# Kernel optimization log

Hardware: AMD Instinct MI355X
Metric: run time of the kernel (lower is better)

The kernel has to match this reference:

```python
import jax, jax.numpy as jnp
import numpy as np

B, S, D, H = 2, 2048, 1024, 16
HD = D // H  # head_dim = 64


def setup_inputs() -> dict:
    key = jax.random.key(0)
    ks = jax.random.split(key, 9)
    s = 1.0 / np.sqrt(D)
    return {
        "x": jax.random.normal(ks[0], (B, S, D), dtype=jnp.float32),
        "Wq": jax.random.uniform(ks[1], (D, D), jnp.float32, -s, s),
        "bq": jnp.zeros((D,), jnp.float32),
        "Wk": jax.random.uniform(ks[2], (D, D), jnp.float32, -s, s),
        "bk": jnp.zeros((D,), jnp.float32),
        "Wv": jax.random.uniform(ks[3], (D, D), jnp.float32, -s, s),
        "bv": jnp.zeros((D,), jnp.float32),
        "Wo": jax.random.uniform(ks[4], (D, D), jnp.float32, -s, s),
        "bo": jnp.zeros((D,), jnp.float32),
    }


def reference(x, Wq, bq, Wk, bk, Wv, bv, Wo, bo):
    # x: [B,S,D] -> Q/K/V: [B,H,S,HD]
    def heads(t):
        return t.reshape(B, S, H, HD).transpose(0, 2, 1, 3)

    Q = heads(x @ Wq + bq)
    K = heads(x @ Wk + bk)
    V = heads(x @ Wv + bv)
    scale = jnp.sqrt(jnp.asarray(HD, dtype=x.dtype))
    energy = jnp.einsum("bhqd,bhkd->bhqk", Q, K) / scale  # [B,H,S,S]
    attn = jax.nn.softmax(energy, axis=-1)
    # dropout is identity in eval mode
    o = jnp.einsum("bhqk,bhkd->bhqd", attn, V)  # [B,H,S,HD]
    o = o.transpose(0, 2, 1, 3).reshape(B, S, D)
    return o @ Wo + bo
```

## Files before the change

### kernel.cpp

```cpp
#include <hip/hip_runtime.h>
#include <hip/hip_bf16.h>

#define B_  2
#define S_  2048
#define D_  1024
#define H_  16
#define HD_ 64

typedef __attribute__((ext_vector_type(8))) short bf16x8;
typedef __attribute__((ext_vector_type(4))) short bf16x4;
typedef __attribute__((ext_vector_type(4))) float f32x4;

typedef __attribute__((address_space(1))) const short gbl_short;
typedef __attribute__((address_space(3))) short lds_short;

__device__ __forceinline__ short f2bf(float f) {
  union { float f; unsigned u; } v; v.f = f;
  unsigned r = (v.u + 0x7FFFu + ((v.u >> 16) & 1u)) >> 16;
  return (short)r;
}

__device__ __forceinline__ short bf16s(float f) {
  __hip_bfloat16 h = __float2bfloat16(f);
  return *reinterpret_cast<short*>(&h);
}

__global__ __launch_bounds__(256) void cast_x_kernel(const float* __restrict__ x,
                                                     short* __restrict__ xb) {
  int i = blockIdx.x * 256 + threadIdx.x;
  float4 v = ((const float4*)x)[i];
  short4 o;
  o.x = f2bf(v.x); o.y = f2bf(v.y); o.z = f2bf(v.z); o.w = f2bf(v.w);
  ((short4*)xb)[i] = o;
}

__global__ __launch_bounds__(256) void transpose_cast_w(
    const float* __restrict__ w0, const float* __restrict__ w1,
    const float* __restrict__ w2, const float* __restrict__ w3,
    short* __restrict__ t0, short* __restrict__ t1,
    short* __restrict__ t2, short* __restrict__ t3) {
  const float* W = blockIdx.z == 0 ? w0 : blockIdx.z == 1 ? w1 : blockIdx.z == 2 ? w2 : w3;
  short* T       = blockIdx.z == 0 ? t0 : blockIdx.z == 1 ? t1 : blockIdx.z == 2 ? t2 : t3;
  __shared__ float tile[32][33];
  int tx = threadIdx.x, ty = threadIdx.y;
  int x0 = blockIdx.x * 32, y0 = blockIdx.y * 32;
#pragma unroll
  for (int i = 0; i < 4; ++i)
    tile[ty + i * 8][tx] = W[(y0 + ty + i * 8) * D_ + x0 + tx];
  __syncthreads();
#pragma unroll
  for (int i = 0; i < 4; ++i)
    T[(x0 + ty + i * 8) * D_ + y0 + tx] = f2bf(tile[tx][ty + i * 8]);
}

__global__ __launch_bounds__(256) void qkv_gemm(
    const short* __restrict__ xb,
    const short* __restrict__ Wqt, const short* __restrict__ Wkt, const short* __restrict__ Wvt,
    const float* __restrict__ bq, const float* __restrict__ bk, const float* __restrict__ bv,
    short* __restrict__ Qb, short* __restrict__ Kb, short* __restrict__ Vtb) {
  const int which = blockIdx.z;
  const short* Bt   = which == 0 ? Wqt : which == 1 ? Wkt : Wvt;
  const float* bias = which == 0 ? bq  : which == 1 ? bk  : bv;
  const float scl   = which == 0 ? 0.125f * 1.44269504089f : 1.0f;
  const int lane = threadIdx.x & 63, wave = threadIdx.x >> 6;
  const int l15 = lane & 15, quad = lane >> 4;
  const int wm = wave & 1, wn = wave >> 1;
  const int m0 = blockIdx.x * 128, n0 = blockIdx.y * 128;
  const int srow = lane >> 2;
  const int skp  = (lane & 3) * 8;

  __shared__ short lA[2][128 * 32];
  __shared__ short lB[2][128 * 32];

  f32x4 acc[4][4];
#pragma unroll
  for (int mi = 0; mi < 4; ++mi)
#pragma unroll
    for (int ni = 0; ni < 4; ++ni) { f32x4 z = {0.f, 0.f, 0.f, 0.f}; acc[mi][ni] = z; }

  auto stage = [&](int it, int buf) {
    int kk = it * 32;
#pragma unroll
    for (int j = 0; j < 2; ++j) {
      int c = wave * 2 + j;
      int row = c * 16 + srow;
      __builtin_amdgcn_global_load_lds(
          (gbl_short*)(xb + (m0 + row) * D_ + kk + skp),
          (lds_short*)(&lA[buf][0] + c * 512 + lane * 8), 16, 0, 0);
      __builtin_amdgcn_global_load_lds(
          (gbl_short*)(Bt + (n0 + row) * D_ + kk + skp),
          (lds_short*)(&lB[buf][0] + c * 512 + lane * 8), 16, 0, 0);
    }
  };

  stage(0, 0);
  __syncthreads();
  for (int it = 0; it < 32; ++it) {
    int cur = it & 1;
    if (it < 31) stage(it + 1, cur ^ 1);
    bf16x8 af[4], bf[4];
#pragma unroll
    for (int i = 0; i < 4; ++i) {
      af[i] = *(const bf16x8*)(&lA[cur][0] + (wm * 64 + i * 16 + l15) * 32 + quad * 8);
      bf[i] = *(const bf16x8*)(&lB[cur][0] + (wn * 64 + i * 16 + l15) * 32 + quad * 8);
    }
#pragma unroll
    for (int mi = 0; mi < 4; ++mi)
#pragma unroll
      for (int ni = 0; ni < 4; ++ni)
        acc[mi][ni] = __builtin_amdgcn_mfma_f32_16x16x32_bf16(af[mi], bf[ni], acc[mi][ni], 0, 0, 0);
    if (it < 31) __syncthreads();
  }

#pragma unroll
  for (int mi = 0; mi < 4; ++mi) {
    int m = m0 + wm * 64 + mi * 16 + quad * 4;
    int bb = m >> 11;
    int s0 = m & (S_ - 1);
#pragma unroll
    for (int ni = 0; ni < 4; ++ni) {
      int n = n0 + wn * 64 + ni * 16 + l15;
      int h = n >> 6, hd = n & 63;
      float bsv = bias[n];
      if (which < 2) {
        short* dst = which == 0 ? Qb : Kb;
#pragma unroll
        for (int r = 0; r < 4; ++r)
          dst[((bb * H_ + h) * S_ + (s0 + r)) * HD_ + hd] = f2bf((acc[mi][ni][r] + bsv) * scl);
      } else {
        short4 pk;
        pk.x = f2bf(acc[mi][ni][0] + bsv);
        pk.y = f2bf(acc[mi][ni][1] + bsv);
        pk.z = f2bf(acc[mi][ni][2] + bsv);
        pk.w = f2bf(acc[mi][ni][3] + bsv);
        *(short4*)(Vtb + ((bb * H_ + h) * HD_ + hd) * S_ + s0) = pk;
      }
    }
  }
}

__global__ __launch_bounds__(256) void out_gemm(
    const short* __restrict__ Ob, const short* __restrict__ Wot,
    const float* __restrict__ bo, float* __restrict__ out) {
  const int lane = threadIdx.x & 63, wave = threadIdx.x >> 6;
  const int l15 = lane & 15, quad = lane >> 4;
  const int m0 = blockIdx.x * 128, n0 = blockIdx.y * 64;
  const int srow = lane >> 2;
  const int skp  = (lane & 3) * 8;

  __shared__ short lA[2][128 * 32];
  __shared__ short lB[2][64 * 32];

  f32x4 acc[2][4];
#pragma unroll
  for (int mi = 0; mi < 2; ++mi)
#pragma unroll
    for (int ni = 0; ni < 4; ++ni) { f32x4 z = {0.f, 0.f, 0.f, 0.f}; acc[mi][ni] = z; }

  auto stage = [&](int it, int buf) {
    int kk = it * 32;
#pragma unroll
    for (int j = 0; j < 2; ++j) {
      int c = wave * 2 + j;
      __builtin_amdgcn_global_load_lds(
          (gbl_short*)(Ob + (m0 + c * 16 + srow) * D_ + kk + skp),
          (lds_short*)(&lA[buf][0] + c * 512 + lane * 8), 16, 0, 0);
    }
    __builtin_amdgcn_global_load_lds(
        (gbl_short*)(Wot + (n0 + wave * 16 + srow) * D_ + kk + skp),
        (lds_short*)(&lB[buf][0] + wave * 512 + lane * 8), 16, 0, 0);
  };

  stage(0, 0);
  __syncthreads();
  for (int it = 0; it < 32; ++it) {
    int cur = it & 1;
    if (it < 31) stage(it + 1, cur ^ 1);
    bf16x8 af[2], bf[4];
#pragma unroll
    for (int i = 0; i < 2; ++i)
      af[i] = *(const bf16x8*)(&lA[cur][0] + (wave * 32 + i * 16 + l15) * 32 + quad * 8);
#pragma unroll
    for (int i = 0; i < 4; ++i)
      bf[i] = *(const bf16x8*)(&lB[cur][0] + (i * 16 + l15) * 32 + quad * 8);
#pragma unroll
    for (int mi = 0; mi < 2; ++mi)
#pragma unroll
      for (int ni = 0; ni < 4; ++ni)
        acc[mi][ni] = __builtin_amdgcn_mfma_f32_16x16x32_bf16(af[mi], bf[ni], acc[mi][ni], 0, 0, 0);
    if (it < 31) __syncthreads();
  }

#pragma unroll
  for (int mi = 0; mi < 2; ++mi) {
    int m = m0 + wave * 32 + mi * 16 + quad * 4;
#pragma unroll
    for (int ni = 0; ni < 4; ++ni) {
      int n = n0 + ni * 16 + l15;
      float bsv = bo[n];
#pragma unroll
      for (int r = 0; r < 4; ++r)
        out[(m + r) * D_ + n] = acc[mi][ni][r] + bsv;
    }
  }
}

__global__ __launch_bounds__(256, 2) void attn_kernel(
    const short* __restrict__ Qb, const short* __restrict__ Kb,
    const short* __restrict__ Vtb, short* __restrict__ Ob) {
  const int qt = blockIdx.x, h = blockIdx.y, b = blockIdx.z;
  const int base = (b * H_ + h) * S_ * HD_;
  const int tid = threadIdx.x;
  const int lane = tid & 63, wave = tid >> 6;
  const int grp = wave >> 1;
  const int wq  = wave & 1;
  const int l15 = lane & 15, quad = lane >> 4;

  __shared__ __align__(16) char smem[33280];
  short* lK = (short*)smem;
  short* lV = (short*)(smem + 16384);

  const int q0 = qt * 128 + wq * 64;

  bf16x8 qf[4][2];
#pragma unroll
  for (int mi = 0; mi < 4; ++mi)
#pragma unroll
    for (int ks = 0; ks < 2; ++ks)
      qf[mi][ks] = *(const bf16x8*)(Qb + base + (q0 + mi * 16 + l15) * HD_ + ks * 32 + quad * 8);

  f32x4 oacc[4][4];
  f32x4 lacc[4];
#pragma unroll
  for (int mi = 0; mi < 4; ++mi) {
    f32x4 z = {0.f, 0.f, 0.f, 0.f};
    lacc[mi] = z;
#pragma unroll
    for (int nb = 0; nb < 4; ++nb) oacc[mi][nb] = z;
  }

  bf16x8 onesf;
#pragma unroll
  for (int i = 0; i < 8; ++i) onesf[i] = (short)0x3F80;

  const int tig = tid & 127;
  const int slotK = tig & 7,  rowK = tig >> 3;
  const int slotV = tig & 3,  rowV = tig >> 2;
  const short* kp = Kb + base + (grp * 1024 + rowK) * HD_ + ((slotK ^ (rowK & 7)) * 8);
  const short* vp = Vtb + base + rowV * S_ + grp * 1024 + ((slotV ^ ((rowV >> 2) & 3)) * 8);
  lds_short* ldk = (lds_short*)(lK + grp * 2048 + tig * 8);
  lds_short* ldv = (lds_short*)(lV + grp * 2048 + tig * 8);

  auto stage = [&](int kt, int buf) {
#pragma unroll
    for (int j = 0; j < 2; ++j) {
      __builtin_amdgcn_global_load_lds((gbl_short*)(kp + kt * 32 * HD_ + j * 16 * HD_),
                                       ldk + buf * 4096 + j * 1024, 16, 0, 0);
      __builtin_amdgcn_global_load_lds((gbl_short*)(vp + kt * 32 + j * 32 * S_),
                                       ldv + buf * 4096 + j * 1024, 16, 0, 0);
    }
  };

  const int swzK = l15 & 7;
  const int fsw  = (l15 >> 2) & 3;
  const int g1 = (quad >> 1) ^ fsw;
  const int g2 = (2 | (quad >> 1)) ^ fsw;
  const int vsub = (quad & 1) * 4;

  stage(0, 0);
  __syncthreads();

  for (int kt = 0; kt < 32; ++kt) {
    const int buf = kt & 1;
    if (kt < 31) stage(kt + 1, buf ^ 1);

    const short* lKc = lK + buf * 4096 + grp * 2048;
    const short* lVc = lV + buf * 4096 + grp * 2048;

    f32x4 sacc[4][2];
#pragma unroll
    for (int mi = 0; mi < 4; ++mi)
#pragma unroll
      for (int nb = 0; nb < 2; ++nb) { f32x4 z = {0.f, 0.f, 0.f, 0.f}; sacc[mi][nb] = z; }
#pragma unroll
    for (int nb = 0; nb < 2; ++nb)
#pragma unroll
      for (int ks = 0; ks < 2; ++ks) {
        bf16x8 kf = *(const bf16x8*)(lKc + (nb * 16 + l15) * 64 + (((ks * 4 + quad) ^ swzK) * 8));
#pragma unroll
        for (int mi = 0; mi < 4; ++mi)
          sacc[mi][nb] = __builtin_amdgcn_mfma_f32_16x16x32_bf16(kf, qf[mi][ks], sacc[mi][nb], 0, 0, 0);
      }

    bf16x8 af[4];
#pragma unroll
    for (int mi = 0; mi < 4; ++mi)
#pragma unroll
      for (int j = 0; j < 8; ++j)
        af[mi][j] = bf16s(__builtin_amdgcn_exp2f(sacc[mi][j >> 2][j & 3]));

#pragma unroll
    for (int nbh = 0; nbh < 4; ++nbh) {
      const short* vrow = lVc + (nbh * 16 + l15) * 32 + vsub;
      bf16x4 v1 = *(const bf16x4*)(vrow + g1 * 8);
      bf16x4 v2 = *(const bf16x4*)(vrow + g2 * 8);
      bf16x8 vf = __builtin_shufflevector(v1, v2, 0, 1, 2, 3, 4, 5, 6, 7);
#pragma unroll
      for (int mi = 0; mi < 4; ++mi)
        oacc[mi][nbh] = __builtin_amdgcn_mfma_f32_16x16x32_bf16(af[mi], vf, oacc[mi][nbh], 0, 0, 0);
    }
#pragma unroll
    for (int mi = 0; mi < 4; ++mi)
      lacc[mi] = __builtin_amdgcn_mfma_f32_16x16x32_bf16(af[mi], onesf, lacc[mi], 0, 0, 0);
    __syncthreads();
  }

  float* exch = (float*)smem;
  float* lex  = (float*)(smem + 32768);
  if (grp == 1) {
#pragma unroll
    for (int mi = 0; mi < 4; ++mi)
#pragma unroll
      for (int nbh = 0; nbh < 4; ++nbh)
#pragma unroll
        for (int r = 0; r < 4; ++r)
          exch[wq * 4096 + (mi * 16 + quad * 4 + r) * 64 + nbh * 16 + l15] = oacc[mi][nbh][r];
    if (l15 == 0) {
#pragma unroll
      for (int mi = 0; mi < 4; ++mi)
#pragma unroll
        for (int r = 0; r < 4; ++r)
          lex[wq * 64 + mi * 16 + quad * 4 + r] = lacc[mi][r];
    }
  }
  __syncthreads();
  if (grp == 0) {
#pragma unroll
    for (int mi = 0; mi < 4; ++mi)
#pragma unroll
      for (int r = 0; r < 4; ++r) {
        int row = mi * 16 + quad * 4 + r;
        float l2 = lex[wq * 64 + row];
        float inv = 1.0f / (lacc[mi][r] + l2);
        int sg = q0 + row;
#pragma unroll
        for (int nbh = 0; nbh < 4; ++nbh) {
          float o2 = exch[wq * 4096 + row * 64 + nbh * 16 + l15];
          Ob[(b * S_ + sg) * D_ + h * HD_ + nbh * 16 + l15] =
              bf16s((oacc[mi][nbh][r] + o2) * inv);
        }
      }
  }
}

extern "C" void kernel_launch(void* const* d_in, const int* in_sizes, int n_in,
                              void* d_out, int out_size, void* d_ws, size_t ws_size,
                              hipStream_t stream) {
  (void)in_sizes; (void)n_in; (void)out_size; (void)ws_size;
  const float* x  = (const float*)d_in[0];
  const float* Wq = (const float*)d_in[1];
  const float* bq = (const float*)d_in[2];
  const float* Wk = (const float*)d_in[3];
  const float* bk = (const float*)d_in[4];
  const float* Wv = (const float*)d_in[5];
  const float* bv = (const float*)d_in[6];
  const float* Wo = (const float*)d_in[7];
  const float* bo = (const float*)d_in[8];
  float* out = (float*)d_out;

  char* ws = (char*)d_ws;
  short* xb  = (short*)(ws);
  short* Wqt = (short*)(ws + 8388608);
  short* Wkt = Wqt + 1048576;
  short* Wvt = Wkt + 1048576;
  short* Wot = Wvt + 1048576;
  short* Qb  = Wot + 1048576;
  short* Kb  = Qb + 4194304;
  short* Vtb = Kb + 4194304;
  short* Ob  = Vtb + 4194304;

  cast_x_kernel<<<4096, 256, 0, stream>>>(x, xb);
  transpose_cast_w<<<dim3(32, 32, 4), dim3(32, 8), 0, stream>>>(
      Wq, Wk, Wv, Wo, Wqt, Wkt, Wvt, Wot);
  qkv_gemm<<<dim3(32, 8, 3), 256, 0, stream>>>(
      xb, Wqt, Wkt, Wvt, bq, bk, bv, Qb, Kb, Vtb);
  attn_kernel<<<dim3(16, 16, 2), 256, 0, stream>>>(Qb, Kb, Vtb, Ob);
  out_gemm<<<dim3(32, 16), 256, 0, stream>>>(Ob, Wot, bo, out);
}
```

Measured before the change: 193.6 us.

## Triple-buffer GEMM LDS stages with XOR swizzle and enlarge out_gemm tile

Both projection GEMMs move from double-buffered LDS staging with __syncthreads to a three-stage ring. Explicit vmcnt waits and raw barriers let two loads stay in flight while compute runs. The k-chunk column index is XOR-swizzled by row bits on write and read to reduce LDS bank conflicts on the 16-byte fragment reads. out_gemm switches from 128x64 to 128x128 tiles with a 2x2 wave layout, which halves its grid and increases reuse. This costs more LDS per block and lower occupancy, and correctness now depends on the hand-counted vmcnt values.

```diff
diff --git a/kernel.cpp b/kernel.cpp
--- a/kernel.cpp
+++ b/kernel.cpp
@@ -67,10 +67,11 @@
   const int wm = wave & 1, wn = wave >> 1;
   const int m0 = blockIdx.x * 128, n0 = blockIdx.y * 128;
   const int srow = lane >> 2;
-  const int skp  = (lane & 3) * 8;
-
-  __shared__ short lA[2][128 * 32];
-  __shared__ short lB[2][128 * 32];
+  const int skp  = (((lane & 3) ^ ((srow >> 1) & 3)) * 8);
+  const int rsw  = (l15 >> 1) & 3;
+
+  __shared__ short lA[3][128 * 32];
+  __shared__ short lB[3][128 * 32];
 
   f32x4 acc[4][4];
 #pragma unroll
@@ -93,24 +94,36 @@
     }
   };
 
-  stage(0, 0);
-  __syncthreads();
-  for (int it = 0; it < 32; ++it) {
-    int cur = it & 1;
-    if (it < 31) stage(it + 1, cur ^ 1);
+  auto compute = [&](int cur) {
     bf16x8 af[4], bf[4];
 #pragma unroll
     for (int i = 0; i < 4; ++i) {
-      af[i] = *(const bf16x8*)(&lA[cur][0] + (wm * 64 + i * 16 + l15) * 32 + quad * 8);
-      bf[i] = *(const bf16x8*)(&lB[cur][0] + (wn * 64 + i * 16 + l15) * 32 + quad * 8);
+      af[i] = *(const bf16x8*)(&lA[cur][0] + (wm * 64 + i * 16 + l15) * 32 + ((quad ^ rsw)) * 8);
+      bf[i] = *(const bf16x8*)(&lB[cur][0] + (wn * 64 + i * 16 + l15) * 32 + ((quad ^ rsw)) * 8);
     }
 #pragma unroll
     for (int mi = 0; mi < 4; ++mi)
 #pragma unroll
       for (int ni = 0; ni < 4; ++ni)
         acc[mi][ni] = __builtin_amdgcn_mfma_f32_16x16x32_bf16(af[mi], bf[ni], acc[mi][ni], 0, 0, 0);
-    if (it < 31) __syncthreads();
-  }
+  };
+
+  stage(0, 0);
+  stage(1, 1);
+  for (int it = 0; it < 30; ++it) {
+    stage(it + 2, (it + 2) % 3);
+    asm volatile("s_waitcnt vmcnt(8)" ::: "memory");
+    __builtin_amdgcn_s_barrier();
+    compute(it % 3);
+    asm volatile("" ::: "memory");
+    __builtin_amdgcn_s_barrier();
+  }
+  asm volatile("s_waitcnt vmcnt(4)" ::: "memory");
+  __builtin_amdgcn_s_barrier();
+  compute(0);
+  asm volatile("s_waitcnt vmcnt(0)" ::: "memory");
+  __builtin_amdgcn_s_barrier();
+  compute(1);
 
 #pragma unroll
   for (int mi = 0; mi < 4; ++mi) {
@@ -144,16 +157,18 @@
     const float* __restrict__ bo, float* __restrict__ out) {
   const int lane = threadIdx.x & 63, wave = threadIdx.x >> 6;
   const int l15 = lane & 15, quad = lane >> 4;
-  const int m0 = blockIdx.x * 128, n0 = blockIdx.y * 64;
+  const int wm = wave & 1, wn = wave >> 1;
+  const int m0 = blockIdx.x * 128, n0 = blockIdx.y * 128;
   const int srow = lane >> 2;
-  const int skp  = (lane & 3) * 8;
-
-  __shared__ short lA[2][128 * 32];
-  __shared__ short lB[2][64 * 32];
-
-  f32x4 acc[2][4];
-#pragma unroll
-  for (int mi = 0; mi < 2; ++mi)
+  const int skp  = (((lane & 3) ^ ((srow >> 1) & 3)) * 8);
+  const int rsw  = (l15 >> 1) & 3;
+
+  __shared__ short lA[3][128 * 32];
+  __shared__ short lB[3][128 * 32];
+
+  f32x4 acc[4][4];
+#pragma unroll
+  for (int mi = 0; mi < 4; ++mi)
 #pragma unroll
     for (int ni = 0; ni < 4; ++ni) { f32x4 z = {0.f, 0.f, 0.f, 0.f}; acc[mi][ni] = z; }
 
@@ -162,41 +177,53 @@
 #pragma unroll
     for (int j = 0; j < 2; ++j) {
       int c = wave * 2 + j;
+      int row = c * 16 + srow;
       __builtin_amdgcn_global_load_lds(
-          (gbl_short*)(Ob + (m0 + c * 16 + srow) * D_ + kk + skp),
+          (gbl_short*)(Ob + (m0 + row) * D_ + kk + skp),
           (lds_short*)(&lA[buf][0] + c * 512 + lane * 8), 16, 0, 0);
-    }
-    __builtin_amdgcn_global_load_lds(
-        (gbl_short*)(Wot + (n0 + wave * 16 + srow) * D_ + kk + skp),
-        (lds_short*)(&lB[buf][0] + wave * 512 + lane * 8), 16, 0, 0);
+      __builtin_amdgcn_global_load_lds(
+          (gbl_short*)(Wot + (n0 + row) * D_ + kk + skp),
+          (lds_short*)(&lB[buf][0] + c * 512 + lane * 8), 16, 0, 0);
+    }
   };
 
-  stage(0, 0);
-  __syncthreads();
-  for (int it = 0; it < 32; ++it) {
-    int cur = it & 1;
-    if (it < 31) stage(it + 1, cur ^ 1);
-    bf16x8 af[2], bf[4];
-#pragma unroll
-    for (int i = 0; i < 2; ++i)
-      af[i] = *(const bf16x8*)(&lA[cur][0] + (wave * 32 + i * 16 + l15) * 32 + quad * 8);
-#pragma unroll
-    for (int i = 0; i < 4; ++i)
-      bf[i] = *(const bf16x8*)(&lB[cur][0] + (i * 16 + l15) * 32 + quad * 8);
-#pragma unroll
-    for (int mi = 0; mi < 2; ++mi)
+  auto compute = [&](int cur) {
+    bf16x8 af[4], bf[4];
+#pragma unroll
+    for (int i = 0; i < 4; ++i) {
+      af[i] = *(const bf16x8*)(&lA[cur][0] + (wm * 64 + i * 16 + l15) * 32 + ((quad ^ rsw)) * 8);
+      bf[i] = *(const bf16x8*)(&lB[cur][0] + (wn * 64 + i * 16 + l15) * 32 + ((quad ^ rsw)) * 8);
+    }
+#pragma unroll
+    for (int mi = 0; mi < 4; ++mi)
 #pragma unroll
       for (int ni = 0; ni < 4; ++ni)
         acc[mi][ni] = __builtin_amdgcn_mfma_f32_16x16x32_bf16(af[mi], bf[ni], acc[mi][ni], 0, 0, 0);
-    if (it < 31) __syncthreads();
-  }
-
-#pragma unroll
-  for (int mi = 0; mi < 2; ++mi) {
-    int m = m0 + wave * 32 + mi * 16 + quad * 4;
+  };
+
+  stage(0, 0);
+  stage(1, 1);
+  for (int it = 0; it < 30; ++it) {
+    stage(it + 2, (it + 2) % 3);
+    asm volatile("s_waitcnt vmcnt(8)" ::: "memory");
+    __builtin_amdgcn_s_barrier();
+    compute(it % 3);
+    asm volatile("" ::: "memory");
+    __builtin_amdgcn_s_barrier();
+  }
+  asm volatile("s_waitcnt vmcnt(4)" ::: "memory");
+  __builtin_amdgcn_s_barrier();
+  compute(0);
+  asm volatile("s_waitcnt vmcnt(0)" ::: "memory");
+  __builtin_amdgcn_s_barrier();
+  compute(1);
+
+#pragma unroll
+  for (int mi = 0; mi < 4; ++mi) {
+    int m = m0 + wm * 64 + mi * 16 + quad * 4;
 #pragma unroll
     for (int ni = 0; ni < 4; ++ni) {
-      int n = n0 + ni * 16 + l15;
+      int n = n0 + wn * 64 + ni * 16 + l15;
       float bsv = bo[n];
 #pragma unroll
       for (int r = 0; r < 4; ++r)
@@ -385,5 +412,5 @@
   qkv_gemm<<<dim3(32, 8, 3), 256, 0, stream>>>(
       xb, Wqt, Wkt, Wvt, bq, bk, bv, Qb, Kb, Vtb);
   attn_kernel<<<dim3(16, 16, 2), 256, 0, stream>>>(Qb, Kb, Vtb, Ob);
-  out_gemm<<<dim3(32, 16), 256, 0, stream>>>(Ob, Wot, bo, out);
-}
+  out_gemm<<<dim3(32, 8), 256, 0, stream>>>(Ob, Wot, bo, out);
+}
```

Result: faster. 188.2 us (-2.8%).
